# Performance work log

Hardware: AMD Instinct MI355X
Metric: run time of the kernel (lower is better)

## Reference

```python
import jax, jax.numpy as jnp
import numpy as np

N_FFT = 1024
HOP = 256
WIN = 1024
N_MELS = 80
SR = 22050
F_MIN = 0.0
CUTOFF = N_FFT // 2 + 1  # 513
PAD = (N_FFT - HOP) // 2  # 384
LOG_CLIP = 1e-5
B, T = 32, 262144


def _hann_periodic(n):
    return (0.5 - 0.5 * np.cos(2.0 * np.pi * np.arange(n) / n)).astype(np.float64)


def _hz_to_mel(f):
    f = np.atleast_1d(np.asarray(f, dtype=np.float64))
    f_sp = 200.0 / 3
    mels = f / f_sp
    min_log_hz = 1000.0
    min_log_mel = min_log_hz / f_sp
    logstep = np.log(6.4) / 27.0
    log_t = f >= min_log_hz
    mels[log_t] = min_log_mel + np.log(f[log_t] / min_log_hz) / logstep
    return mels


def _mel_to_hz(m):
    m = np.asarray(m, dtype=np.float64)
    f_sp = 200.0 / 3
    freqs = m * f_sp
    min_log_hz = 1000.0
    min_log_mel = min_log_hz / f_sp
    logstep = np.log(6.4) / 27.0
    log_t = m >= min_log_mel
    freqs = np.where(log_t, min_log_hz * np.exp(logstep * (m - min_log_mel)), freqs)
    return freqs


def _mel_filterbank(sr, n_fft, n_mels, fmin, fmax):
    # librosa.filters.mel with htk=False, norm='slaney'
    if fmax is None:
        fmax = sr / 2.0
    mel_f = _mel_to_hz(np.linspace(_hz_to_mel(fmin)[0], _hz_to_mel(fmax)[0], n_mels + 2))
    fftfreqs = np.linspace(0.0, sr / 2.0, 1 + n_fft // 2)
    fdiff = np.diff(mel_f)
    ramps = mel_f[:, None] - fftfreqs[None, :]
    lower = -ramps[:-2] / fdiff[:-1, None]
    upper = ramps[2:] / fdiff[1:, None]
    weights = np.maximum(0.0, np.minimum(lower, upper))
    enorm = 2.0 / (mel_f[2:n_mels + 2] - mel_f[:n_mels])
    weights *= enorm[:, None]
    return weights.astype(np.float32)  # [n_mels, cutoff]


def _forward_basis():
    # Windowed real/imag DFT basis, as in the torch module.
    fourier = np.fft.fft(np.eye(N_FFT))
    basis = np.vstack([np.real(fourier[:CUTOFF, :]), np.imag(fourier[:CUTOFF, :])])
    basis = basis * _hann_periodic(WIN)[None, :]
    return basis.astype(np.float32)  # [2*cutoff, n_fft]


def setup_inputs() -> dict:
    key = jax.random.key(0)
    audio = jax.random.uniform(key, (B, T), dtype=jnp.float32, minval=-1.0, maxval=1.0)
    return {
        "audio": audio,
        "forward_basis": jnp.asarray(_forward_basis()),
        "mel_basis": jnp.asarray(_mel_filterbank(SR, N_FFT, N_MELS, F_MIN, None)),
        "jitter_steps": 0,
    }


def reference(audio, forward_basis, mel_basis, jitter_steps):
    # jitter_steps == 0 at eval: no random shift applied.
    padded = jnp.pad(audio, ((0, 0), (PAD, PAD)), mode="reflect")  # [B, T+2*PAD]
    n_frames = (padded.shape[-1] - N_FFT) // HOP + 1
    idx = jnp.arange(n_frames)[:, None] * HOP + jnp.arange(N_FFT)[None, :]
    frames = padded[:, idx]  # [B, n_frames, n_fft]
    ft = jnp.einsum("btn,cn->bct", frames, forward_basis)  # [B, 2*cutoff, n_frames]
    real, imag = ft[:, :CUTOFF, :], ft[:, CUTOFF:, :]
    mag = jnp.sqrt(real * real + imag * imag)  # [B, cutoff, n_frames]
    mel = jnp.einsum("mc,bct->bmt", mel_basis, mag)  # [B, n_mels, n_frames]
    return jnp.log(jnp.clip(mel, LOG_CLIP, None))
```

## Files before the change

kernel.cpp:

```cpp
#include <hip/hip_runtime.h>
#include <hip/hip_bf16.h>

typedef short bf16x8 __attribute__((ext_vector_type(8)));
typedef float f32x4  __attribute__((ext_vector_type(4)));
typedef int   i32x4  __attribute__((ext_vector_type(4)));

#define T_AUDIO 262144
#define PADL 384
#define CUTOFF 513
#define CPAD 576
#define NMELS 80
#define PCH 16448
#define PBYTES (PCH*16)
#define EB64 17152

__device__ __forceinline__ unsigned short f2bf(float f){
  union { float f; unsigned u; } v; v.f = f;
  return (unsigned short)((v.u + 0x7FFFu + ((v.u >> 16) & 1u)) >> 16);
}
__device__ __forceinline__ float bf2f(unsigned short u){
  union { unsigned u; float f; } v; v.u = (unsigned)u << 16; return v.f;
}

__device__ __forceinline__ void gload_lds16(const void* g, void* l){
  __builtin_amdgcn_global_load_lds(
      (const __attribute__((address_space(1))) unsigned int*)g,
      (__attribute__((address_space(3))) unsigned int*)l, 16, 0, 0);
}

__global__ void k_audio(const float* __restrict__ audio, unsigned short* __restrict__ planes){
  int bx = blockIdx.x;
  int b  = bx / 65;
  int ci = (bx % 65) * 256 + threadIdx.x;
  if (ci >= PCH) return;
  const float* ap = audio + (long)b * T_AUDIO;
  int s0 = 16 * ci - 384;
  float v[16];
  if (s0 >= 0 && s0 + 15 < T_AUDIO){
    #pragma unroll
    for (int q = 0; q < 4; ++q){
      f32x4 a = *(const f32x4*)(ap + s0 + q * 4);
      v[q*4]=a[0]; v[q*4+1]=a[1]; v[q*4+2]=a[2]; v[q*4+3]=a[3];
    }
  } else {
    #pragma unroll
    for (int e = 0; e < 16; ++e){
      int s = s0 + e;
      if (s < 0) s = -s;
      if (s >= T_AUDIO) s = 2*(T_AUDIO-1) - s;
      v[e] = ap[s];
    }
  }
  bf16x8 ev, ov;
  #pragma unroll
  for (int e = 0; e < 8; ++e){
    ev[e] = (short)f2bf(v[2*e]);
    ov[e] = (short)f2bf(v[2*e+1]);
  }
  unsigned short* pE = planes + (long)b * 2 * (PCH * 8);
  *(bf16x8*)(pE + (long)ci * 8)            = ev;
  *(bf16x8*)(pE + PCH * 8 + (long)ci * 8)  = ov;
}

__global__ void k_basis4(const float* __restrict__ basis, unsigned short* __restrict__ bi2f){
  int CI = blockIdx.x * 256 + threadIdx.x;
  int l  = CI & 63;
  int f  = (CI >> 6) & 7;
  int s  = (CI >> 9) & 15;
  int p  = (CI >> 13) & 1;
  int g  = CI >> 14;
  int R  = g * 128 + (f >> 2) * 64 + (f & 3) * 16 + (l & 15);
  int srcr = (R >> 1) + 513 * (R & 1);
  const float* sp = basis + srcr * 1024 + 2 * (s * 32 + (l >> 4) * 8) + p;
  bf16x8 o;
  #pragma unroll
  for (int e = 0; e < 8; ++e) o[e] = (short)f2bf(sp[2*e]);
  *(bf16x8*)(bi2f + (long)CI * 8) = o;
}

__global__ void k_w(const float* __restrict__ w, const float* __restrict__ basis,
                    unsigned short* __restrict__ wb, float* __restrict__ beo){
  int gid = blockIdx.x * 256 + threadIdx.x;
  if (gid < NMELS * CPAD){
    int m = gid / CPAD, p = gid % CPAD;
    float v = 0.f;
    if (p <= 256) v = w[m * CUTOFF + p];
    else if (p >= 264 && p <= 519) v = w[m * CUTOFF + (p - 7)];
    wb[gid] = f2bf(v);
  } else {
    int g2 = gid - NMELS * CPAD;
    int par = g2 >> 9, m = g2 & 511;
    beo[g2] = par ? basis[769 * 1024 + 2*m + 1] : basis[256 * 1024 + 2*m];
  }
}

__global__ void k_extra(const unsigned short* __restrict__ planes,
                        const float* __restrict__ beo,
                        unsigned short* __restrict__ magT){
  int tid = threadIdx.x, l = tid & 63, w = tid >> 6;
  long fr = (long)blockIdx.x * 4 + w;
  int b = (int)(fr >> 10), t = (int)(fr & 1023);
  const unsigned short* pE = planes + (long)b * 2 * (PCH * 8);
  const unsigned short* pO = pE + PCH * 8;
  int idx = t * 128 + l * 8;
  bf16x8 ev = *(const bf16x8*)(pE + idx);
  bf16x8 ov = *(const bf16x8*)(pO + idx);
  f32x4 be0 = *(const f32x4*)(beo + l*8);
  f32x4 be1 = *(const f32x4*)(beo + l*8 + 4);
  f32x4 bo0 = *(const f32x4*)(beo + 512 + l*8);
  f32x4 bo1 = *(const f32x4*)(beo + 512 + l*8 + 4);
  float re = bf2f(ev[0])*be0[0] + bf2f(ev[1])*be0[1] + bf2f(ev[2])*be0[2] + bf2f(ev[3])*be0[3]
           + bf2f(ev[4])*be1[0] + bf2f(ev[5])*be1[1] + bf2f(ev[6])*be1[2] + bf2f(ev[7])*be1[3];
  float im = bf2f(ov[0])*bo0[0] + bf2f(ov[1])*bo0[1] + bf2f(ov[2])*bo0[2] + bf2f(ov[3])*bo0[3]
           + bf2f(ov[4])*bo1[0] + bf2f(ov[5])*bo1[1] + bf2f(ov[6])*bo1[2] + bf2f(ov[7])*bo1[3];
  #pragma unroll
  for (int m = 1; m < 64; m <<= 1){
    re += __shfl_xor(re, m, 64);
    im += __shfl_xor(im, m, 64);
  }
  long tg = fr * CPAD;
  if (l == 0) magT[tg + 256] = f2bf(sqrtf(re*re + im*im));
  if (l < 63){
    int p = (l < 7) ? (257 + l) : (513 + l);
    magT[tg + p] = 0;
  }
}

__launch_bounds__(256, 4)
__global__ void k_stft(const unsigned short* __restrict__ bi2f,
                       const unsigned short* __restrict__ planes,
                       unsigned short* __restrict__ magT){
  __shared__ __align__(16) char LDS[2 * EB64];
  const int tid = threadIdx.x;
  const int l   = tid & 63, w = tid >> 6;
  const int x   = l & 15, h = l >> 4;

  int bx = blockIdx.x;
  int sw = ((bx & 7) << 8) | (bx >> 3);
  const int g    = sw & 3;
  const int nt64 = sw >> 2;

  {
    const char* pb = (const char*)planes + (long)(nt64 >> 4) * 2 * PBYTES;
    const int kto = (nt64 & 15) * 1024;
    #pragma unroll
    for (int it = 0; it < 5; ++it){
      int o = it * 256 + tid;
      if (o < 1072){
        long so = (long)((o ^ ((o >> 4) & 15)) + kto) * 16;
        gload_lds16(pb + so,          LDS + o * 16);
        gload_lds16(pb + PBYTES + so, LDS + EB64 + o * 16);
      }
    }
  }
  asm volatile("s_waitcnt vmcnt(0)" ::: "memory");
  __syncthreads();

  const char* Ab = (const char*)bi2f + (long)(g * 256 + 2 * w) * 1024 + l * 16;

  int C0[4];
  #pragma unroll
  for (int j = 0; j < 4; ++j) C0[j] = (j * 16 + x) * 16 + h;

  f32x4 accE[2][4] = {}, accO[2][4] = {};

  #pragma unroll
  for (int s = 0; s < 16; ++s){
    bf16x8 aE0 = *(const bf16x8*)(Ab + s * 8192);
    bf16x8 aE1 = *(const bf16x8*)(Ab + s * 8192 + 1024);
    bf16x8 aO0 = *(const bf16x8*)(Ab + 131072 + s * 8192);
    bf16x8 aO1 = *(const bf16x8*)(Ab + 131072 + s * 8192 + 1024);
    bf16x8 bqE[4], bqO[4];
    #pragma unroll
    for (int j = 0; j < 4; ++j){
      int C = C0[j] + s * 4; int ad = (C ^ ((C >> 4) & 15)) << 4;
      bqE[j] = *(const bf16x8*)(LDS + ad);
      bqO[j] = *(const bf16x8*)(LDS + EB64 + ad);
    }
    __builtin_amdgcn_s_setprio(1);
    #pragma unroll
    for (int j = 0; j < 4; ++j){
      accE[0][j] = __builtin_amdgcn_mfma_f32_16x16x32_bf16(aE0, bqE[j], accE[0][j], 0, 0, 0);
      accE[1][j] = __builtin_amdgcn_mfma_f32_16x16x32_bf16(aE1, bqE[j], accE[1][j], 0, 0, 0);
    }
    #pragma unroll
    for (int j = 0; j < 4; ++j){
      accO[0][j] = __builtin_amdgcn_mfma_f32_16x16x32_bf16(aO0, bqO[j], accO[0][j], 0, 0, 0);
      accO[1][j] = __builtin_amdgcn_mfma_f32_16x16x32_bf16(aO1, bqO[j], accO[1][j], 0, 0, 0);
    }
    __builtin_amdgcn_s_setprio(0);
  }

  __syncthreads();
  #pragma unroll
  for (int i = 0; i < 2; ++i){
    int cp1 = w * 8 + i * 4 + h;
    int sm  = 63 - cp1;
    #pragma unroll
    for (int j = 0; j < 4; ++j){
      int tl = j * 16 + x;
      f32x4 E = accE[i][j], O = accO[i][j];
      float m1 = sqrtf((E[0]+O[0])*(E[0]+O[0]) + (E[1]+O[1])*(E[1]+O[1]));
      float m2 = sqrtf((E[2]+O[2])*(E[2]+O[2]) + (E[3]+O[3])*(E[3]+O[3]));
      float m3 = sqrtf((E[0]-O[0])*(E[0]-O[0]) + (E[1]-O[1])*(E[1]-O[1]));
      float m4 = sqrtf((E[2]-O[2])*(E[2]-O[2]) + (E[3]-O[3])*(E[3]-O[3]));
      unsigned p1 = (unsigned)f2bf(m1) | ((unsigned)f2bf(m2) << 16);
      unsigned p2 = (unsigned)f2bf(m4) | ((unsigned)f2bf(m3) << 16);
      int xs = (tl & 7) << 2;
      *(unsigned*)(LDS + tl * 256 + ((cp1 ^ xs) << 2)) = p1;
      *(unsigned*)(LDS + tl * 256 + ((sm  ^ xs) << 2)) = p2;
    }
  }
  __syncthreads();

  {
    const long rowbase = (long)(nt64 * 64) * CPAD;
    int grp = tid & 15, rr = tid >> 4;
    int cb0 = (grp < 8) ? (g * 64 + grp * 8) : (456 - 64 * g + (grp - 8) * 8);
    #pragma unroll
    for (int pass = 0; pass < 4; ++pass){
      int tl = pass * 16 + rr;
      int f4 = (grp * 4) ^ ((tl & 7) << 2);
      i32x4 vv = *(const i32x4*)(LDS + tl * 256 + f4 * 4);
      *(i32x4*)((char*)magT + (rowbase + (long)tl * CPAD + cb0) * 2) = vv;
    }
  }
}

__launch_bounds__(256)
__global__ void k_mel(const unsigned short* __restrict__ wb,
                      const unsigned short* __restrict__ magT,
                      float* __restrict__ out){
  __shared__ unsigned short Ws[80 * 32];
  __shared__ unsigned short Ms[128 * 32];
  int tid  = threadIdx.x, lane = tid & 63, wid = tid >> 6;
  int bx   = blockIdx.x;
  int bt   = bx & 7, b = bx >> 3;
  int t0   = bt * 128;
  f32x4 acc[5][2] = {};
  const char* Mb = (const char*)(magT + ((long)b * 1024 + t0) * CPAD);
  const char* Wb = (const char*)wb;

  for (int kt = 0; kt < 18; ++kt){
    int k0b = kt * 64;
    {
      int o = tid * 16;
      gload_lds16(Wb + (o >> 6) * 1152 + k0b + (o & 63), (char*)Ws + wid * 1024);
      if (wid == 0){
        int o2 = 4096 + lane * 16;
        gload_lds16(Wb + (o2 >> 6) * 1152 + k0b + (o2 & 63), (char*)Ws + 4096);
      }
    }
    #pragma unroll
    for (int q = 0; q < 2; ++q){
      int o = (q * 256 + tid) * 16;
      gload_lds16(Mb + (long)(o >> 6) * 1152 + k0b + (o & 63), (char*)Ms + q * 4096 + wid * 1024);
    }
    __syncthreads();
    bf16x8 af[5], bfr[2];
    int kb = (lane >> 4) << 4;
    #pragma unroll
    for (int i = 0; i < 5; ++i)
      af[i] = *(const bf16x8*)((const char*)Ws + (i*16 + (lane & 15)) * 64 + kb);
    #pragma unroll
    for (int j = 0; j < 2; ++j)
      bfr[j] = *(const bf16x8*)((const char*)Ms + (wid*32 + j*16 + (lane & 15)) * 64 + kb);
    #pragma unroll
    for (int i = 0; i < 5; ++i)
      #pragma unroll
      for (int j = 0; j < 2; ++j)
        acc[i][j] = __builtin_amdgcn_mfma_f32_16x16x32_bf16(af[i], bfr[j], acc[i][j], 0, 0, 0);
    __syncthreads();
  }
  #pragma unroll
  for (int i = 0; i < 5; ++i)
    #pragma unroll
    for (int j = 0; j < 2; ++j){
      int m = i*16 + ((lane >> 4) << 2);
      int t = t0 + wid*32 + j*16 + (lane & 15);
      #pragma unroll
      for (int r = 0; r < 4; ++r){
        float v = acc[i][j][r];
        out[((long)b * NMELS + (m + r)) * 1024 + t] = logf(fmaxf(v, 1e-5f));
      }
    }
}

__global__ void k_sentinel(float* out, int n){
  int i = blockIdx.x * 256 + threadIdx.x;
  if (i < n) out[i] = 12345.0f;
}

extern "C" void kernel_launch(void* const* d_in, const int* in_sizes, int n_in,
                              void* d_out, int out_size, void* d_ws, size_t ws_size,
                              hipStream_t stream){
  const float* audio = (const float*)d_in[0];
  const float* basis = (const float*)d_in[1];
  const float* melw  = (const float*)d_in[2];
  float* out = (float*)d_out;

  size_t off_bi  = 0;
  size_t off_wb  = (size_t)1024 * 1024;
  size_t off_beo = off_wb + (size_t)NMELS * CPAD * 2;
  size_t off_mag = off_beo + 1024 * 4;
  size_t off_pl  = off_mag + (size_t)32 * 1024 * CPAD * 2;
  size_t total   = off_pl + (size_t)32 * 2 * PBYTES;

  if (ws_size < total){
    k_sentinel<<<(out_size + 255) / 256, 256, 0, stream>>>(out, out_size);
    return;
  }
  char* ws = (char*)d_ws;
  unsigned short* bi2f   = (unsigned short*)(ws + off_bi);
  unsigned short* wb     = (unsigned short*)(ws + off_wb);
  float*          beo    = (float*)(ws + off_beo);
  unsigned short* magT   = (unsigned short*)(ws + off_mag);
  unsigned short* planes = (unsigned short*)(ws + off_pl);

  k_audio <<< 2080, 256, 0, stream>>>(audio, planes);
  k_basis4<<<  256, 256, 0, stream>>>(basis, bi2f);
  k_w     <<<  184, 256, 0, stream>>>(melw, basis, wb, beo);
  k_extra <<< 8192, 256, 0, stream>>>(planes, beo, magT);
  k_stft  <<< 2048, 256, 0, stream>>>(bi2f, planes, magT);
  k_mel   <<<  256, 256, 0, stream>>>(wb, magT, out);
}
```

Baseline: 77.76 us.

## Merge prep kernels, move pad zeroing into STFT, halve mel tile for more blocks

Combines the basis and mel-weight prep kernels into one launch. The zero-padding writes for magT move from the scattered per-lane stores in k_extra into k_stft's coalesced LDS-staged store, with a wider LDS row stride. The mel GEMM uses 64-frame tiles (512 blocks instead of 256) with an XOR-swizzled LDS layout to cut bank conflicts and raise occupancy. This adds extra store work to some STFT blocks and reorders k_extra after k_stft, so it must not overwrite column 256.

Result: no change. 78.21 us (+0.6%).

```diff
diff --git a/kernel.cpp b/kernel.cpp
--- a/kernel.cpp
+++ b/kernel.cpp
@@ -62,35 +62,37 @@
   *(bf16x8*)(pE + PCH * 8 + (long)ci * 8)  = ov;
 }
 
-__global__ void k_basis4(const float* __restrict__ basis, unsigned short* __restrict__ bi2f){
-  int CI = blockIdx.x * 256 + threadIdx.x;
-  int l  = CI & 63;
-  int f  = (CI >> 6) & 7;
-  int s  = (CI >> 9) & 15;
-  int p  = (CI >> 13) & 1;
-  int g  = CI >> 14;
-  int R  = g * 128 + (f >> 2) * 64 + (f & 3) * 16 + (l & 15);
-  int srcr = (R >> 1) + 513 * (R & 1);
-  const float* sp = basis + srcr * 1024 + 2 * (s * 32 + (l >> 4) * 8) + p;
-  bf16x8 o;
-  #pragma unroll
-  for (int e = 0; e < 8; ++e) o[e] = (short)f2bf(sp[2*e]);
-  *(bf16x8*)(bi2f + (long)CI * 8) = o;
-}
-
-__global__ void k_w(const float* __restrict__ w, const float* __restrict__ basis,
-                    unsigned short* __restrict__ wb, float* __restrict__ beo){
-  int gid = blockIdx.x * 256 + threadIdx.x;
-  if (gid < NMELS * CPAD){
-    int m = gid / CPAD, p = gid % CPAD;
-    float v = 0.f;
-    if (p <= 256) v = w[m * CUTOFF + p];
-    else if (p >= 264 && p <= 519) v = w[m * CUTOFF + (p - 7)];
-    wb[gid] = f2bf(v);
+__global__ void k_prep(const float* __restrict__ basis, const float* __restrict__ w,
+                       unsigned short* __restrict__ bi2f, unsigned short* __restrict__ wb,
+                       float* __restrict__ beo){
+  int bx = blockIdx.x, tid = threadIdx.x;
+  if (bx < 256){
+    int CI = bx * 256 + tid;
+    int l  = CI & 63;
+    int f  = (CI >> 6) & 7;
+    int s  = (CI >> 9) & 15;
+    int p  = (CI >> 13) & 1;
+    int g  = CI >> 14;
+    int R  = g * 128 + (f >> 2) * 64 + (f & 3) * 16 + (l & 15);
+    int srcr = (R >> 1) + 513 * (R & 1);
+    const float* sp = basis + srcr * 1024 + 2 * (s * 32 + (l >> 4) * 8) + p;
+    bf16x8 o;
+    #pragma unroll
+    for (int e = 0; e < 8; ++e) o[e] = (short)f2bf(sp[2*e]);
+    *(bf16x8*)(bi2f + (long)CI * 8) = o;
   } else {
-    int g2 = gid - NMELS * CPAD;
-    int par = g2 >> 9, m = g2 & 511;
-    beo[g2] = par ? basis[769 * 1024 + 2*m + 1] : basis[256 * 1024 + 2*m];
+    int gid = (bx - 256) * 256 + tid;
+    if (gid < NMELS * CPAD){
+      int m = gid / CPAD, p = gid % CPAD;
+      float v = 0.f;
+      if (p <= 256) v = w[m * CUTOFF + p];
+      else if (p >= 264 && p <= 519) v = w[m * CUTOFF + (p - 7)];
+      wb[gid] = f2bf(v);
+    } else if (gid < NMELS * CPAD + 1024){
+      int g2 = gid - NMELS * CPAD;
+      int par = g2 >> 9, m = g2 & 511;
+      beo[g2] = par ? basis[769 * 1024 + 2*m + 1] : basis[256 * 1024 + 2*m];
+    }
   }
 }
 
@@ -118,12 +120,7 @@
     re += __shfl_xor(re, m, 64);
     im += __shfl_xor(im, m, 64);
   }
-  long tg = fr * CPAD;
-  if (l == 0) magT[tg + 256] = f2bf(sqrtf(re*re + im*im));
-  if (l < 63){
-    int p = (l < 7) ? (257 + l) : (513 + l);
-    magT[tg + p] = 0;
-  }
+  if (l == 0) magT[fr * CPAD + 256] = f2bf(sqrtf(re*re + im*im));
 }
 
 __launch_bounds__(256, 4)
@@ -192,6 +189,17 @@
   }
 
   __syncthreads();
+  if (g == 0){
+    #pragma unroll
+    for (int z = 0; z < 7; ++z){
+      int id = z * 256 + tid;
+      int tl = id / 28, sl = 64 + id % 28;
+      *(unsigned*)(LDS + tl * 384 + sl * 4) = 0;
+    }
+  } else if (g == 3){
+    int tl = tid >> 2, sl = 64 + (tid & 3);
+    *(unsigned*)(LDS + tl * 384 + sl * 4) = 0;
+  }
   #pragma unroll
   for (int i = 0; i < 2; ++i){
     int cp1 = w * 8 + i * 4 + h;
@@ -207,22 +215,28 @@
       unsigned p1 = (unsigned)f2bf(m1) | ((unsigned)f2bf(m2) << 16);
       unsigned p2 = (unsigned)f2bf(m4) | ((unsigned)f2bf(m3) << 16);
       int xs = (tl & 7) << 2;
-      *(unsigned*)(LDS + tl * 256 + ((cp1 ^ xs) << 2)) = p1;
-      *(unsigned*)(LDS + tl * 256 + ((sm  ^ xs) << 2)) = p2;
+      *(unsigned*)(LDS + tl * 384 + ((cp1 ^ xs) << 2)) = p1;
+      *(unsigned*)(LDS + tl * 384 + ((sm  ^ xs) << 2)) = p2;
     }
   }
   __syncthreads();
 
   {
     const long rowbase = (long)(nt64 * 64) * CPAD;
-    int grp = tid & 15, rr = tid >> 4;
-    int cb0 = (grp < 8) ? (g * 64 + grp * 8) : (456 - 64 * g + (grp - 8) * 8);
-    #pragma unroll
-    for (int pass = 0; pass < 4; ++pass){
-      int tl = pass * 16 + rr;
-      int f4 = (grp * 4) ^ ((tl & 7) << 2);
-      i32x4 vv = *(const i32x4*)(LDS + tl * 256 + f4 * 4);
-      *(i32x4*)((char*)magT + (rowbase + (long)tl * CPAD + cb0) * 2) = vv;
+    int grp = tid & 31, rr = tid >> 5;
+    int ngrp = (g == 0) ? 23 : (g == 3) ? 17 : 16;
+    int cb0;
+    if (grp < 8)       cb0 = g * 64 + grp * 8;
+    else if (grp < 16) cb0 = 456 - 64 * g + (grp - 8) * 8;
+    else               cb0 = ((g == 0) ? 520 : 256) + (grp - 16) * 8;
+    #pragma unroll
+    for (int pass = 0; pass < 8; ++pass){
+      int tl = pass * 8 + rr;
+      if (grp < ngrp){
+        int f4 = (grp < 16) ? ((grp * 4) ^ ((tl & 7) << 2)) : (grp * 4);
+        i32x4 vv = *(const i32x4*)(LDS + tl * 384 + f4 * 4);
+        *(i32x4*)((char*)magT + (rowbase + (long)tl * CPAD + cb0) * 2) = vv;
+      }
     }
   }
 }
@@ -232,58 +246,57 @@
                       const unsigned short* __restrict__ magT,
                       float* __restrict__ out){
   __shared__ unsigned short Ws[80 * 32];
-  __shared__ unsigned short Ms[128 * 32];
-  int tid  = threadIdx.x, lane = tid & 63, wid = tid >> 6;
-  int bx   = blockIdx.x;
-  int bt   = bx & 7, b = bx >> 3;
-  int t0   = bt * 128;
-  f32x4 acc[5][2] = {};
+  __shared__ unsigned short Ms[64 * 32];
+  int tid = threadIdx.x, l = tid & 63, w = tid >> 6;
+  int x = l & 15, h = l >> 4;
+  int bx = blockIdx.x;
+  int bt = bx & 15, b = bx >> 4;
+  int t0 = bt * 64;
+  f32x4 acc[5] = {};
   const char* Mb = (const char*)(magT + ((long)b * 1024 + t0) * CPAD);
   const char* Wb = (const char*)wb;
 
   for (int kt = 0; kt < 18; ++kt){
     int k0b = kt * 64;
     {
-      int o = tid * 16;
-      gload_lds16(Wb + (o >> 6) * 1152 + k0b + (o & 63), (char*)Ws + wid * 1024);
-      if (wid == 0){
-        int o2 = 4096 + lane * 16;
-        gload_lds16(Wb + (o2 >> 6) * 1152 + k0b + (o2 & 63), (char*)Ws + 4096);
+      int pl = tid >> 3, sl = (tid & 7) ^ (pl & 7);
+      gload_lds16(Wb + (pl * 2 + (sl >> 2)) * 1152 + k0b + (sl & 3) * 16, (char*)Ws + tid * 16);
+      if (w == 0){
+        int d2 = 256 + l;
+        int pl2 = d2 >> 3, sl2 = (d2 & 7) ^ (pl2 & 7);
+        gload_lds16(Wb + (pl2 * 2 + (sl2 >> 2)) * 1152 + k0b + (sl2 & 3) * 16, (char*)Ws + d2 * 16);
       }
     }
-    #pragma unroll
-    for (int q = 0; q < 2; ++q){
-      int o = (q * 256 + tid) * 16;
-      gload_lds16(Mb + (long)(o >> 6) * 1152 + k0b + (o & 63), (char*)Ms + q * 4096 + wid * 1024);
+    {
+      int pl = tid >> 3, sl = (tid & 7) ^ (pl & 7);
+      gload_lds16(Mb + (long)(pl * 2 + (sl >> 2)) * 1152 + k0b + (sl & 3) * 16, (char*)Ms + tid * 16);
     }
     __syncthreads();
-    bf16x8 af[5], bfr[2];
-    int kb = (lane >> 4) << 4;
+    bf16x8 af[5], bfr;
+    #pragma unroll
+    for (int i = 0; i < 5; ++i){
+      int row = i * 16 + x;
+      int pl = row >> 1, sl = (((row & 1) << 2) + h) ^ (pl & 7);
+      af[i] = *(const bf16x8*)((const char*)Ws + pl * 128 + sl * 16);
+    }
+    {
+      int row = w * 16 + x;
+      int pl = row >> 1, sl = (((row & 1) << 2) + h) ^ (pl & 7);
+      bfr = *(const bf16x8*)((const char*)Ms + pl * 128 + sl * 16);
+    }
     #pragma unroll
     for (int i = 0; i < 5; ++i)
-      af[i] = *(const bf16x8*)((const char*)Ws + (i*16 + (lane & 15)) * 64 + kb);
-    #pragma unroll
-    for (int j = 0; j < 2; ++j)
-      bfr[j] = *(const bf16x8*)((const char*)Ms + (wid*32 + j*16 + (lane & 15)) * 64 + kb);
-    #pragma unroll
-    for (int i = 0; i < 5; ++i)
-      #pragma unroll
-      for (int j = 0; j < 2; ++j)
-        acc[i][j] = __builtin_amdgcn_mfma_f32_16x16x32_bf16(af[i], bfr[j], acc[i][j], 0, 0, 0);
+      acc[i] = __builtin_amdgcn_mfma_f32_16x16x32_bf16(af[i], bfr, acc[i], 0, 0, 0);
     __syncthreads();
   }
-  #pragma unroll
-  for (int i = 0; i < 5; ++i)
-    #pragma unroll
-    for (int j = 0; j < 2; ++j){
-      int m = i*16 + ((lane >> 4) << 2);
-      int t = t0 + wid*32 + j*16 + (lane & 15);
-      #pragma unroll
-      for (int r = 0; r < 4; ++r){
-        float v = acc[i][j][r];
-        out[((long)b * NMELS + (m + r)) * 1024 + t] = logf(fmaxf(v, 1e-5f));
-      }
-    }
+  int t = t0 + w * 16 + x;
+  #pragma unroll
+  for (int i = 0; i < 5; ++i){
+    int m = i * 16 + (h << 2);
+    #pragma unroll
+    for (int r = 0; r < 4; ++r)
+      out[((long)b * NMELS + (m + r)) * 1024 + t] = logf(fmaxf(acc[i][r], 1e-5f));
+  }
 }
 
 __global__ void k_sentinel(float* out, int n){
@@ -317,10 +330,9 @@
   unsigned short* magT   = (unsigned short*)(ws + off_mag);
   unsigned short* planes = (unsigned short*)(ws + off_pl);
 
+  k_prep  <<<  440, 256, 0, stream>>>(basis, melw, bi2f, wb, beo);
   k_audio <<< 2080, 256, 0, stream>>>(audio, planes);
-  k_basis4<<<  256, 256, 0, stream>>>(basis, bi2f);
-  k_w     <<<  184, 256, 0, stream>>>(melw, basis, wb, beo);
+  k_stft  <<< 2048, 256, 0, stream>>>(bi2f, planes, magT);
   k_extra <<< 8192, 256, 0, stream>>>(planes, beo, magT);
-  k_stft  <<< 2048, 256, 0, stream>>>(bi2f, planes, magT);
-  k_mel   <<<  256, 256, 0, stream>>>(wb, magT, out);
-}
+  k_mel   <<<  512, 256, 0, stream>>>(wb, magT, out);
+}
```
